# Kernel optimization log

Hardware: AMD Instinct MI355X
Metric: run time of the kernel (lower is better)

The kernel has to match this reference:

```python
import jax, jax.numpy as jnp
import numpy as np
from jax import lax

BN_EPS = 1e-5


def ste_sign(t):
    # sign() binarization with straight-through estimator (identity grad),
    # matching BinarizeConv2d which binarizes .data in-place.
    return t + lax.stop_gradient(jnp.sign(t) - t)


def setup_inputs() -> dict:
    key = jax.random.key(0)
    k1, k2, k3, k4 = jax.random.split(key, 4)
    N, C, H, W = 128, 256, 28, 28
    x = jax.random.normal(k1, (N, C, H, W), dtype=jnp.float32)
    w = jax.random.normal(k2, (C, C, 3, 3), dtype=jnp.float32)  # OIHW
    gamma = jnp.ones((C,), dtype=jnp.float32)
    beta = jnp.zeros((C,), dtype=jnp.float32)
    running_mean = jax.random.normal(k3, (C,), dtype=jnp.float32)
    running_var = jax.random.uniform(k4, (C,), dtype=jnp.float32)
    return {"x": x, "w": w, "gamma": gamma, "beta": beta,
            "running_mean": running_mean, "running_var": running_var}


def reference(x, w, gamma, beta, running_mean, running_var):
    residual = x
    # Binarize activations and weights to {-1, 0, +1} via sign (0 measure-zero for randn)
    xb = ste_sign(x)
    wb = ste_sign(w)
    # 3x3 conv, stride 1, padding 1, no bias
    out = lax.conv_general_dilated(
        xb, wb, window_strides=(1, 1), padding=((1, 1), (1, 1)),
        dimension_numbers=("NCHW", "OIHW", "NCHW"))
    # BatchNorm2d (inference form with running stats), per-channel affine
    inv = gamma / jnp.sqrt(running_var + BN_EPS)  # [C]
    out = out * inv[None, :, None, None] + (beta - running_mean * inv)[None, :, None, None]
    # Hardtanh
    out = jnp.clip(out, -1.0, 1.0)
    # residual add (downsample is None)
    return out + residual
```

## Files before the change

kernel.cpp:

```cpp
#include <hip/hip_runtime.h>
#include <stdint.h>

typedef unsigned long long u64;

#define N_ 128
#define C_ 256
#define H_ 28
#define W_ 28
#define BN_EPS_ 1e-5f

__global__ __launch_bounds__(256) void pack_x_kernel(const float* __restrict__ x,
                                                     u64* __restrict__ xbits) {
    int tid = blockIdx.x * blockDim.x + threadIdx.x;
    if (tid >= N_ * H_ * W_) return;
    int w  = tid % W_;
    int hn = tid / W_;
    int h  = hn % H_;
    int n  = hn / H_;
    const float* xp = x + ((size_t)n * C_ * H_ * W_) + (size_t)h * W_ + w;
    u64 b0 = 0, b1 = 0, b2 = 0, b3 = 0;
    #pragma unroll 8
    for (int c = 0; c < 64; ++c) {
        b0 |= (u64)(xp[(size_t)(c      ) * (H_ * W_)] < 0.f) << c;
        b1 |= (u64)(xp[(size_t)(c +  64) * (H_ * W_)] < 0.f) << c;
        b2 |= (u64)(xp[(size_t)(c + 128) * (H_ * W_)] < 0.f) << c;
        b3 |= (u64)(xp[(size_t)(c + 192) * (H_ * W_)] < 0.f) << c;
    }
    u64* dst = xbits + (size_t)tid * 4;
    dst[0] = b0; dst[1] = b1; dst[2] = b2; dst[3] = b3;
}

__global__ __launch_bounds__(256) void pack_w_kernel(const float* __restrict__ w,
                                                     u64* __restrict__ wbits) {
    int gid  = blockIdx.x * blockDim.x + threadIdx.x;
    int wave = gid >> 6;
    int lane = gid & 63;
    if (wave >= C_ * 9 * 4) return;
    int k    = wave & 3;
    int rest = wave >> 2;
    int tap  = rest % 9;
    int co   = rest / 9;
    int ci   = k * 64 + lane;
    float val = w[((size_t)co * C_ + ci) * 9 + tap];
    u64 mask = __ballot(val < 0.f);
    if (lane == 0) wbits[wave] = mask;
}

__global__ __launch_bounds__(256) void conv_kernel(
    const u64* __restrict__ xbits, const u64* __restrict__ wbits,
    const float* __restrict__ x,
    const float* __restrict__ gamma, const float* __restrict__ beta,
    const float* __restrict__ mean, const float* __restrict__ var,
    float* __restrict__ out) {
    int nh = blockIdx.x;
    int h  = nh % H_;
    int n  = nh / H_;
    int co = threadIdx.x;

    float inv  = gamma[co] / sqrtf(var[co] + BN_EPS_);
    float bias = beta[co] - mean[co] * inv;

    u64 wr[9][4];
    {
        const ulonglong2* wp = (const ulonglong2*)wbits + (size_t)co * 18;
        #pragma unroll
        for (int i = 0; i < 9; ++i) {
            ulonglong2 a = wp[i * 2];
            ulonglong2 b = wp[i * 2 + 1];
            wr[i][0] = a.x; wr[i][1] = a.y; wr[i][2] = b.x; wr[i][3] = b.y;
        }
    }

    __shared__ u64 lx[3][W_][4];
    for (int i = threadIdx.x; i < 3 * W_ * 4; i += 256) {
        int k    = i & 3;
        int rest = i >> 2;
        int ww   = rest % W_;
        int r    = rest / W_;
        int ih   = h - 1 + r;
        u64 v = 0;
        if (ih >= 0 && ih < H_)
            v = xbits[(((size_t)n * H_ + ih) * W_ + ww) * 4 + k];
        lx[r][ww][k] = v;
    }
    __syncthreads();

    const float* xrow = x   + (((size_t)n * C_ + co) * H_ + h) * W_;
    float*       orow = out + (((size_t)n * C_ + co) * H_ + h) * W_;

    int dh0 = (h == 0)      ? 1 : 0;
    int dh1 = (h == H_ - 1) ? 1 : 2;

    for (int wq = 0; wq < W_ / 4; ++wq) {
        float4 res = ((const float4*)xrow)[wq];
        float4 o;
        float*       op = &o.x;
        const float* rp = &res.x;
        #pragma unroll
        for (int j = 0; j < 4; ++j) {
            int wpos = wq * 4 + j;
            int acc = 0;
            int nv  = 0;
            #pragma unroll
            for (int dh = 0; dh < 3; ++dh) {
                if (dh < dh0 || dh > dh1) continue;
                #pragma unroll
                for (int dw = 0; dw < 3; ++dw) {
                    int iw = wpos - 1 + dw;
                    if (iw < 0 || iw >= W_) continue;
                    nv += C_;
                    const u64* xx = lx[dh][iw];
                    const u64* wt = wr[dh * 3 + dw];
                    acc += __popcll(xx[0] ^ wt[0]) + __popcll(xx[1] ^ wt[1]) +
                           __popcll(xx[2] ^ wt[2]) + __popcll(xx[3] ^ wt[3]);
                }
            }
            float convv = (float)(nv - 2 * acc);
            float val   = convv * inv + bias;
            val = fminf(1.f, fmaxf(-1.f, val));
            op[j] = val + rp[j];
        }
        ((float4*)orow)[wq] = o;
    }
}

extern "C" void kernel_launch(void* const* d_in, const int* in_sizes, int n_in,
                              void* d_out, int out_size, void* d_ws, size_t ws_size,
                              hipStream_t stream) {
    const float* x     = (const float*)d_in[0];
    const float* w     = (const float*)d_in[1];
    const float* gamma = (const float*)d_in[2];
    const float* beta  = (const float*)d_in[3];
    const float* mean  = (const float*)d_in[4];
    const float* var   = (const float*)d_in[5];
    float* out = (float*)d_out;

    u64* xbits = (u64*)d_ws;
    u64* wbits = xbits + (size_t)N_ * H_ * W_ * 4;

    int npix = N_ * H_ * W_;
    pack_x_kernel<<<(npix + 255) / 256, 256, 0, stream>>>(x, xbits);
    pack_w_kernel<<<(C_ * 9 * 4 * 64) / 256, 256, 0, stream>>>(w, wbits);
    conv_kernel<<<N_ * H_, 256, 0, stream>>>(xbits, wbits, x, gamma, beta, mean, var, out);
}
```

Baseline: 353.2 us.

## Coalesce bit-packing, reuse input columns across taps, stage output through shared memory

```diff
diff --git a/kernel.cpp b/kernel.cpp
--- a/kernel.cpp
+++ b/kernel.cpp
@@ -11,23 +11,24 @@
 
 __global__ __launch_bounds__(256) void pack_x_kernel(const float* __restrict__ x,
                                                      u64* __restrict__ xbits) {
-    int tid = blockIdx.x * blockDim.x + threadIdx.x;
-    if (tid >= N_ * H_ * W_) return;
-    int w  = tid % W_;
-    int hn = tid / W_;
-    int h  = hn % H_;
-    int n  = hn / H_;
-    const float* xp = x + ((size_t)n * C_ * H_ * W_) + (size_t)h * W_ + w;
-    u64 b0 = 0, b1 = 0, b2 = 0, b3 = 0;
-    #pragma unroll 8
-    for (int c = 0; c < 64; ++c) {
-        b0 |= (u64)(xp[(size_t)(c      ) * (H_ * W_)] < 0.f) << c;
-        b1 |= (u64)(xp[(size_t)(c +  64) * (H_ * W_)] < 0.f) << c;
-        b2 |= (u64)(xp[(size_t)(c + 128) * (H_ * W_)] < 0.f) << c;
-        b3 |= (u64)(xp[(size_t)(c + 192) * (H_ * W_)] < 0.f) << c;
+    int gid  = blockIdx.x * blockDim.x + threadIdx.x;
+    int wave = gid >> 6;
+    int lane = gid & 63;
+    int k    = wave & 3;
+    int nh   = wave >> 2;
+    if (nh >= N_ * H_) return;
+    int h = nh % H_;
+    int n = nh / H_;
+    int c = k * 64 + lane;
+    const float* xp = x + (((size_t)n * C_ + c) * H_ + h) * W_;
+
+    u64 my = 0;
+    #pragma unroll
+    for (int w = 0; w < W_; ++w) {
+        u64 mask = __ballot(xp[w] < 0.f);
+        if (lane == w) my = mask;
     }
-    u64* dst = xbits + (size_t)tid * 4;
-    dst[0] = b0; dst[1] = b1; dst[2] = b2; dst[3] = b3;
+    if (lane < W_) xbits[((size_t)nh * W_ + lane) * 4 + k] = my;
 }
 
 __global__ __launch_bounds__(256) void pack_w_kernel(const float* __restrict__ w,
@@ -57,6 +58,11 @@
     int n  = nh / H_;
     int co = threadIdx.x;
 
+    __shared__ union {
+        u64   lx[3][W_][4];
+        float sout[C_][29];
+    } sm;
+
     float inv  = gamma[co] / sqrtf(var[co] + BN_EPS_);
     float bias = beta[co] - mean[co] * inv;
 
@@ -71,7 +77,6 @@
         }
     }
 
-    __shared__ u64 lx[3][W_][4];
     for (int i = threadIdx.x; i < 3 * W_ * 4; i += 256) {
         int k    = i & 3;
         int rest = i >> 2;
@@ -81,46 +86,59 @@
         u64 v = 0;
         if (ih >= 0 && ih < H_)
             v = xbits[(((size_t)n * H_ + ih) * W_ + ww) * 4 + k];
-        lx[r][ww][k] = v;
+        sm.lx[r][ww][k] = v;
     }
     __syncthreads();
 
-    const float* xrow = x   + (((size_t)n * C_ + co) * H_ + h) * W_;
-    float*       orow = out + (((size_t)n * C_ + co) * H_ + h) * W_;
+    const bool row0 = (h > 0);
+    const bool row2 = (h < H_ - 1);
+    const int  nrows = 1 + (row0 ? 1 : 0) + (row2 ? 1 : 0);
 
-    int dh0 = (h == 0)      ? 1 : 0;
-    int dh1 = (h == H_ - 1) ? 1 : 2;
+    int sacc[W_];
+    int pm = 0, pc = 0;
 
-    for (int wq = 0; wq < W_ / 4; ++wq) {
-        float4 res = ((const float4*)xrow)[wq];
-        float4 o;
-        float*       op = &o.x;
-        const float* rp = &res.x;
-        #pragma unroll
-        for (int j = 0; j < 4; ++j) {
-            int wpos = wq * 4 + j;
-            int acc = 0;
-            int nv  = 0;
-            #pragma unroll
-            for (int dh = 0; dh < 3; ++dh) {
-                if (dh < dh0 || dh > dh1) continue;
-                #pragma unroll
-                for (int dw = 0; dw < 3; ++dw) {
-                    int iw = wpos - 1 + dw;
-                    if (iw < 0 || iw >= W_) continue;
-                    nv += C_;
-                    const u64* xx = lx[dh][iw];
-                    const u64* wt = wr[dh * 3 + dw];
-                    acc += __popcll(xx[0] ^ wt[0]) + __popcll(xx[1] ^ wt[1]) +
-                           __popcll(xx[2] ^ wt[2]) + __popcll(xx[3] ^ wt[3]);
-                }
-            }
-            float convv = (float)(nv - 2 * acc);
-            float val   = convv * inv + bias;
-            val = fminf(1.f, fmaxf(-1.f, val));
-            op[j] = val + rp[j];
-        }
-        ((float4*)orow)[wq] = o;
+    for (int iw = 0; iw < W_; ++iw) {
+        int a0 = 0, a1 = 0, a2 = 0;
+        u64 xw0, xw1, xw2, xw3;
+        #define TAPROW(r, wb)                                                  \
+            xw0 = sm.lx[r][iw][0]; xw1 = sm.lx[r][iw][1];                      \
+            xw2 = sm.lx[r][iw][2]; xw3 = sm.lx[r][iw][3];                      \
+            a0 += __popcll(xw0 ^ wr[wb+0][0]) + __popcll(xw1 ^ wr[wb+0][1]) +  \
+                  __popcll(xw2 ^ wr[wb+0][2]) + __popcll(xw3 ^ wr[wb+0][3]);   \
+            a1 += __popcll(xw0 ^ wr[wb+1][0]) + __popcll(xw1 ^ wr[wb+1][1]) +  \
+                  __popcll(xw2 ^ wr[wb+1][2]) + __popcll(xw3 ^ wr[wb+1][3]);   \
+            a2 += __popcll(xw0 ^ wr[wb+2][0]) + __popcll(xw1 ^ wr[wb+2][1]) +  \
+                  __popcll(xw2 ^ wr[wb+2][2]) + __popcll(xw3 ^ wr[wb+2][3]);
+        if (row0) { TAPROW(0, 0) }
+        { TAPROW(1, 3) }
+        if (row2) { TAPROW(2, 6) }
+        #undef TAPROW
+        if (iw >= 1) sacc[iw - 1] = pm + a2;
+        pm = pc + a1;
+        pc = a0;
+    }
+    sacc[W_ - 1] = pm;
+
+    __syncthreads();
+
+    #pragma unroll
+    for (int w = 0; w < W_; ++w) {
+        int ncols = 3 - (w == 0 ? 1 : 0) - (w == W_ - 1 ? 1 : 0);
+        int nv    = C_ * nrows * ncols;
+        float convv = (float)(nv - 2 * sacc[w]);
+        float val   = convv * inv + bias;
+        val = fminf(1.f, fmaxf(-1.f, val));
+        sm.sout[co][w] = val;
+    }
+    __syncthreads();
+
+    const float* xplane = x   + ((size_t)n * C_ * H_ + h) * W_;
+    float*       oplane = out + ((size_t)n * C_ * H_ + h) * W_;
+    for (int i = threadIdx.x; i < C_ * W_; i += 256) {
+        int c    = i / W_;
+        int wpos = i - c * W_;
+        size_t g = (size_t)c * (H_ * W_) + wpos;
+        oplane[g] = sm.sout[c][wpos] + xplane[g];
     }
 }
 
@@ -138,8 +156,8 @@
     u64* xbits = (u64*)d_ws;
     u64* wbits = xbits + (size_t)N_ * H_ * W_ * 4;
 
-    int npix = N_ * H_ * W_;
-    pack_x_kernel<<<(npix + 255) / 256, 256, 0, stream>>>(x, xbits);
+    int pack_x_threads = N_ * H_ * 4 * 64;
+    pack_x_kernel<<<(pack_x_threads + 255) / 256, 256, 0, stream>>>(x, xbits);
     pack_w_kernel<<<(C_ * 9 * 4 * 64) / 256, 256, 0, stream>>>(w, wbits);
     conv_kernel<<<N_ * H_, 256, 0, stream>>>(xbits, wbits, x, gamma, beta, mean, var, out);
 }
```

Result: faster. 325.7 us (-7.8%).
